# Kernel optimization log

Hardware: AMD Instinct MI355X
Metric: run time of the kernel (lower is better)

Reference implementation:

```python
import jax, jax.numpy as jnp
import numpy as np

NUM_NODES = 100000
HIDDEN = 128
NUM_EDGES = 800000


def setup_inputs() -> dict:
    key = jax.random.key(0)
    ks = jax.random.split(key, 8)
    s = 1.0 / np.sqrt(HIDDEN)

    def lin_w(k):
        return jax.random.uniform(k, (HIDDEN, HIDDEN), minval=-s, maxval=s, dtype=jnp.float32)

    return {
        "node_id": jnp.arange(NUM_NODES, dtype=jnp.int64) if jax.config.jax_enable_x64 else jnp.arange(NUM_NODES, dtype=jnp.int32),
        "edge_index": jax.random.randint(ks[0], (2, NUM_EDGES), 0, NUM_NODES),
        "emb": jax.random.normal(ks[1], (NUM_NODES, HIDDEN), dtype=jnp.float32),
        "W1l": lin_w(ks[2]), "b1l": jnp.zeros((HIDDEN,), jnp.float32), "W1r": lin_w(ks[3]),
        "W2l": lin_w(ks[4]), "b2l": jnp.zeros((HIDDEN,), jnp.float32), "W2r": lin_w(ks[5]),
        "W3l": lin_w(ks[6]), "b3l": jnp.zeros((HIDDEN,), jnp.float32), "W3r": lin_w(ks[7]),
    }


def reference(node_id, edge_index, emb, W1l, b1l, W1r, W2l, b2l, W2r, W3l, b3l, W3r):
    # x: [N, H] node features from embedding lookup
    x = emb[node_id]
    src, dst = edge_index[0], edge_index[1]

    # in-degree per target node (PyG mean aggregation; zero-degree -> 0 output)
    deg = jax.ops.segment_sum(jnp.ones((NUM_EDGES,), x.dtype), dst, num_segments=NUM_NODES)
    inv_deg = 1.0 / jnp.maximum(deg, 1.0)  # [N]

    def sage_conv(h, Wl, bl, Wr):
        # gather source features [E, H], scatter-sum at targets, then mean
        aggr = jax.ops.segment_sum(h[src], dst, num_segments=NUM_NODES) * inv_deg[:, None]
        # out = lin_l(aggr) + lin_r(h); lin_l has bias, lin_r has none (PyG defaults)
        return aggr @ Wl.T + bl + h @ Wr.T

    x = jax.nn.relu(sage_conv(x, W1l, b1l, W1r))
    # dropout p=0.2 with training=False is identity (eval mode)
    x = jax.nn.relu(sage_conv(x, W2l, b2l, W2r))
    return sage_conv(x, W3l, b3l, W3r)
```

## Files before the change

kernel.cpp:

```cpp
#include <hip/hip_runtime.h>

#define H 128

typedef float v4f __attribute__((ext_vector_type(4)));
typedef short v8s __attribute__((ext_vector_type(8)));


__device__ inline unsigned short bf16_rne(float x) {
  unsigned u = __builtin_bit_cast(unsigned, x);
  unsigned r = u + 0x7FFF + ((u >> 16) & 1);
  return (unsigned short)(r >> 16);
}

__device__ inline void split_bf16(float x, unsigned short& hi, unsigned short& lo) {
  unsigned u = __builtin_bit_cast(unsigned, x);
  unsigned r = u + 0x7FFF + ((u >> 16) & 1);
  hi = (unsigned short)(r >> 16);
  float hf = __builtin_bit_cast(float, r & 0xFFFF0000u);
  float d = x - hf;
  unsigned ud = __builtin_bit_cast(unsigned, d);
  unsigned rd = ud + 0x7FFF + ((ud >> 16) & 1);
  lo = (unsigned short)(rd >> 16);
}


__global__ void hist_kernel(const int* __restrict__ dst, int* __restrict__ deg, int E) {
  int e = blockIdx.x * 256 + threadIdx.x;
  if (e < E) atomicAdd(&deg[dst[e]], 1);
}

__global__ __launch_bounds__(1024) void scan1_kernel(const int* __restrict__ deg,
                                                     int* __restrict__ incl,
                                                     int* __restrict__ blk_sum, int N) {
  __shared__ int lds[1024];
  int t = threadIdx.x;
  int i = blockIdx.x * 1024 + t;
  int v = (i < N) ? deg[i] : 0;
  lds[t] = v;
  __syncthreads();
  for (int off = 1; off < 1024; off <<= 1) {
    int x = (t >= off) ? lds[t - off] : 0;
    __syncthreads();
    lds[t] += x;
    __syncthreads();
  }
  if (i < N) incl[i] = lds[t];
  if (t == 1023) blk_sum[blockIdx.x] = lds[1023];
}

__global__ void scan2_kernel(const int* __restrict__ blk_sum, int* __restrict__ blk_off, int B) {
  __shared__ int lds[256];
  int t = threadIdx.x;
  int v = (t < B) ? blk_sum[t] : 0;
  lds[t] = v;
  __syncthreads();
  for (int off = 1; off < 256; off <<= 1) {
    int x = (t >= off) ? lds[t - off] : 0;
    __syncthreads();
    lds[t] += x;
    __syncthreads();
  }
  blk_off[t] = lds[t] - v;
}

__global__ void rowstart_kernel(const int* __restrict__ incl, const int* __restrict__ deg,
                                const int* __restrict__ blk_off, int* __restrict__ row_start,
                                int N) {
  int i = blockIdx.x * 256 + threadIdx.x;
  if (i < N) row_start[i] = blk_off[i >> 10] + incl[i] - deg[i];
}

__global__ void fill_kernel(const int* __restrict__ src, const int* __restrict__ dst,
                            const int* __restrict__ row_start, int* __restrict__ cursor,
                            int* __restrict__ csr_src, int E) {
  int e = blockIdx.x * 256 + threadIdx.x;
  if (e < E) {
    int d = dst[e];
    int p = atomicAdd(&cursor[d], 1);
    csr_src[row_start[d] + p] = src[e];
  }
}


__global__ void gather_kernel(const float* __restrict__ emb, const int* __restrict__ node_id,
                              float* __restrict__ h, unsigned short* __restrict__ hb, int N) {
  int i = blockIdx.x * 256 + threadIdx.x;
  if (i < N * 32) {
    int n = i >> 5, q = i & 31;
    float4 v = ((const float4*)emb)[(size_t)node_id[n] * 32 + q];
    ((float4*)h)[(size_t)n * 32 + q] = v;
    unsigned b0 = bf16_rne(v.x), b1 = bf16_rne(v.y), b2 = bf16_rne(v.z), b3 = bf16_rne(v.w);
    *(uint2*)(hb + (size_t)n * H + q * 4) = make_uint2(b0 | (b1 << 16), b2 | (b3 << 16));
  }
}


__global__ void wsplit_kernel(const float* __restrict__ W0, const float* __restrict__ W1,
                              const float* __restrict__ W2, const float* __restrict__ W3,
                              const float* __restrict__ W4, const float* __restrict__ W5,
                              unsigned short* __restrict__ hi, unsigned short* __restrict__ lo) {
  int i = blockIdx.x * 256 + threadIdx.x;
  int plane = i >> 12;
  int e = (i & 4095) * 4;
  const float* src = plane == 0 ? W0 : plane == 1 ? W1 : plane == 2 ? W2
                   : plane == 3 ? W3 : plane == 4 ? W4 : W5;
  float4 v = *(const float4*)(src + e);
  float vv[4] = {v.x, v.y, v.z, v.w};
  unsigned short hs[4], ls[4];
#pragma unroll
  for (int k = 0; k < 4; ++k) split_bf16(vv[k], hs[k], ls[k]);
  size_t base = (size_t)plane * 16384 + e;
  *(uint2*)(&hi[base]) = make_uint2((unsigned)hs[0] | ((unsigned)hs[1] << 16),
                                    (unsigned)hs[2] | ((unsigned)hs[3] << 16));
  *(uint2*)(&lo[base]) = make_uint2((unsigned)ls[0] | ((unsigned)ls[1] << 16),
                                    (unsigned)ls[2] | ((unsigned)ls[3] << 16));
}


__global__ __launch_bounds__(256) void aggregate_kernel(const unsigned short* __restrict__ hb,
                                                        const int* __restrict__ csr_src,
                                                        const int* __restrict__ row_start,
                                                        const int* __restrict__ deg,
                                                        float* __restrict__ aggr, int N) {
  int node = blockIdx.x * 4 + (threadIdx.x >> 6);
  if (node >= N) return;
  int lane = threadIdx.x & 63;
  int qe = lane >> 4;
  int cl = lane & 15;
  const uint4* __restrict__ h16 = (const uint4*)hb;

  int start = row_start[node];
  int d = deg[node];

  float acc[8] = {0.f, 0.f, 0.f, 0.f, 0.f, 0.f, 0.f, 0.f};

  auto accum = [&](uint4 u) {
    unsigned uu[4] = {u.x, u.y, u.z, u.w};
#pragma unroll
    for (int j = 0; j < 4; ++j) {
      acc[2 * j] += __builtin_bit_cast(float, uu[j] << 16);
      acc[2 * j + 1] += __builtin_bit_cast(float, uu[j] & 0xFFFF0000u);
    }
  };

  int e = qe;
  for (; e + 4 < d; e += 8) {
    int s0 = csr_src[start + e];
    int s1 = csr_src[start + e + 4];
    uint4 u0 = h16[(size_t)s0 * 16 + cl];
    uint4 u1 = h16[(size_t)s1 * 16 + cl];
    accum(u0);
    accum(u1);
  }
  for (; e < d; e += 4) {
    int s = csr_src[start + e];
    accum(h16[(size_t)s * 16 + cl]);
  }

#pragma unroll
  for (int j = 0; j < 8; ++j) {
    acc[j] += __shfl_xor(acc[j], 16);
    acc[j] += __shfl_xor(acc[j], 32);
  }

  float inv = 1.0f / fmaxf((float)d, 1.0f);
  if (qe == 0) {
    *(float4*)(aggr + (size_t)node * H + cl * 8) =
        make_float4(acc[0] * inv, acc[1] * inv, acc[2] * inv, acc[3] * inv);
  } else if (qe == 1) {
    *(float4*)(aggr + (size_t)node * H + cl * 8 + 4) =
        make_float4(acc[4] * inv, acc[5] * inv, acc[6] * inv, acc[7] * inv);
  }
}


template <int RELU>
__global__ __launch_bounds__(256) void gemm_mfma(const float* __restrict__ aggr,
                                                 const float* h,
                                                 const unsigned short* __restrict__ Wl_hi,
                                                 const unsigned short* __restrict__ Wl_lo,
                                                 const unsigned short* __restrict__ Wr_hi,
                                                 const unsigned short* __restrict__ Wr_lo,
                                                 const float* __restrict__ bias,
                                                 float* out, unsigned short* hb_out, int N) {
  __shared__ __align__(16) unsigned short Ah[4096];
  __shared__ __align__(16) unsigned short Al[4096];
  __shared__ __align__(16) unsigned short Wh[4096];
  __shared__ __align__(16) unsigned short Wl_[4096];

  int tid = threadIdx.x;
  int wave = tid >> 6, lane = tid & 63;
  int m = lane & 15, q = lane >> 4;
  int block_row = blockIdx.x * 128;

  v4f acc[16];
#pragma unroll
  for (int t = 0; t < 16; ++t) acc[t] = (v4f){0.f, 0.f, 0.f, 0.f};

  for (int side = 0; side < 2; ++side) {
    const float* X = side ? h : aggr;
    const unsigned short* WH = side ? Wr_hi : Wl_hi;
    const unsigned short* WL = side ? Wr_lo : Wl_lo;

    for (int kb = 0; kb < 4; ++kb) {
      __syncthreads();

#pragma unroll
      for (int p = 0; p < 4; ++p) {
        int s = p * 256 + tid;
        int row = s >> 3;
        int g = s & 7;
        int grow = block_row + row;
        if (grow >= N) grow = N - 1;
        float4 v = *(const float4*)(X + (size_t)grow * H + kb * 32 + g * 4);
        float vv[4] = {v.x, v.y, v.z, v.w};
        unsigned short hs[4], ls[4];
#pragma unroll
        for (int k = 0; k < 4; ++k) split_bf16(vv[k], hs[k], ls[k]);
        int off = (row >> 4) * 512 + (((g >> 1) * 16) + (row & 15)) * 8 + (g & 1) * 4;
        *(uint2*)(&Ah[off]) = make_uint2((unsigned)hs[0] | ((unsigned)hs[1] << 16),
                                         (unsigned)hs[2] | ((unsigned)hs[3] << 16));
        *(uint2*)(&Al[off]) = make_uint2((unsigned)ls[0] | ((unsigned)ls[1] << 16),
                                         (unsigned)ls[2] | ((unsigned)ls[3] << 16));
      }

#pragma unroll
      for (int p = 0; p < 2; ++p) {
        int s = p * 256 + tid;
        int row = s >> 2;
        int g2 = s & 3;
        size_t gsrc = (size_t)row * H + kb * 32 + g2 * 8;
        v8s wh = *(const v8s*)(WH + gsrc);
        v8s wl = *(const v8s*)(WL + gsrc);
        int off = (row >> 4) * 512 + (g2 * 16 + (row & 15)) * 8;
        *(v8s*)(&Wh[off]) = wh;
        *(v8s*)(&Wl_[off]) = wl;
      }

      __syncthreads();

      const v8s* AhF = (const v8s*)Ah;
      const v8s* AlF = (const v8s*)Al;
      const v8s* WhF = (const v8s*)Wh;
      const v8s* WlF = (const v8s*)Wl_;
      v8s ah0 = AhF[(wave * 2 + 0) * 64 + lane];
      v8s ah1 = AhF[(wave * 2 + 1) * 64 + lane];
      v8s al0 = AlF[(wave * 2 + 0) * 64 + lane];
      v8s al1 = AlF[(wave * 2 + 1) * 64 + lane];
#pragma unroll
      for (int c = 0; c < 8; ++c) {
        v8s bh = WhF[c * 64 + lane];
        v8s bl = WlF[c * 64 + lane];
        acc[c] = __builtin_amdgcn_mfma_f32_16x16x32_bf16(ah0, bh, acc[c], 0, 0, 0);
        acc[c] = __builtin_amdgcn_mfma_f32_16x16x32_bf16(al0, bh, acc[c], 0, 0, 0);
        acc[c] = __builtin_amdgcn_mfma_f32_16x16x32_bf16(ah0, bl, acc[c], 0, 0, 0);
        acc[8 + c] = __builtin_amdgcn_mfma_f32_16x16x32_bf16(ah1, bh, acc[8 + c], 0, 0, 0);
        acc[8 + c] = __builtin_amdgcn_mfma_f32_16x16x32_bf16(al1, bh, acc[8 + c], 0, 0, 0);
        acc[8 + c] = __builtin_amdgcn_mfma_f32_16x16x32_bf16(ah1, bl, acc[8 + c], 0, 0, 0);
      }
    }
  }

  float bv[8];
#pragma unroll
  for (int c = 0; c < 8; ++c) bv[c] = bias[c * 16 + m];
#pragma unroll
  for (int tr = 0; tr < 2; ++tr) {
#pragma unroll
    for (int c = 0; c < 8; ++c) {
      v4f a = acc[tr * 8 + c];
#pragma unroll
      for (int i = 0; i < 4; ++i) {
        int row = block_row + wave * 32 + tr * 16 + q * 4 + i;
        if (row < N) {
          float v = a[i] + bv[c];
          if (RELU) v = fmaxf(v, 0.f);
          out[(size_t)row * H + c * 16 + m] = v;
          if (hb_out) hb_out[(size_t)row * H + c * 16 + m] = bf16_rne(v);
        }
      }
    }
  }
}


extern "C" void kernel_launch(void* const* d_in, const int* in_sizes, int n_in,
                              void* d_out, int out_size, void* d_ws, size_t ws_size,
                              hipStream_t stream) {
  const int* node_id = (const int*)d_in[0];
  const int* edge_index = (const int*)d_in[1];
  const float* emb = (const float*)d_in[2];
  const float* W1l = (const float*)d_in[3];
  const float* b1l = (const float*)d_in[4];
  const float* W1r = (const float*)d_in[5];
  const float* W2l = (const float*)d_in[6];
  const float* b2l = (const float*)d_in[7];
  const float* W2r = (const float*)d_in[8];
  const float* W3l = (const float*)d_in[9];
  const float* b3l = (const float*)d_in[10];
  const float* W3r = (const float*)d_in[11];

  int N = in_sizes[0];
  int E = in_sizes[1] / 2;
  const int* src = edge_index;
  const int* dst = edge_index + E;

  char* w = (char*)d_ws;
  auto alloc = [&](size_t bytes) {
    void* p = (void*)w;
    w += (bytes + 255) & ~(size_t)255;
    return p;
  };
  int* deg = (int*)alloc((size_t)N * 4);
  int* cursor = (int*)alloc((size_t)N * 4);
  int* row_start = (int*)alloc((size_t)N * 4);
  int* incl = (int*)alloc((size_t)N * 4);
  int* blk_sum = (int*)alloc(1024);
  int* blk_off = (int*)alloc(1024);
  int* csr_src = (int*)alloc((size_t)E * 4);
  float* hbuf = (float*)alloc((size_t)N * H * 4);
  float* aggr = (float*)alloc((size_t)N * H * 4);
  unsigned short* hb = (unsigned short*)alloc((size_t)N * H * 2);
  unsigned short* whi = (unsigned short*)alloc(6 * 16384 * 2);
  unsigned short* wlo = (unsigned short*)alloc(6 * 16384 * 2);

  hipMemsetAsync(deg, 0, (size_t)N * 4, stream);
  hipMemsetAsync(cursor, 0, (size_t)N * 4, stream);

  hist_kernel<<<(E + 255) / 256, 256, 0, stream>>>(dst, deg, E);
  int SB = (N + 1023) / 1024;
  scan1_kernel<<<SB, 1024, 0, stream>>>(deg, incl, blk_sum, N);
  scan2_kernel<<<1, 256, 0, stream>>>(blk_sum, blk_off, SB);
  rowstart_kernel<<<(N + 255) / 256, 256, 0, stream>>>(incl, deg, blk_off, row_start, N);
  fill_kernel<<<(E + 255) / 256, 256, 0, stream>>>(src, dst, row_start, cursor, csr_src, E);

  gather_kernel<<<(N * 32 + 255) / 256, 256, 0, stream>>>(emb, node_id, hbuf, hb, N);
  wsplit_kernel<<<96, 256, 0, stream>>>(W1l, W1r, W2l, W2r, W3l, W3r, whi, wlo);

  int gag = (N + 3) / 4;
  int ggm = (N + 127) / 128;

  aggregate_kernel<<<gag, 256, 0, stream>>>(hb, csr_src, row_start, deg, aggr, N);
  gemm_mfma<1><<<ggm, 256, 0, stream>>>(aggr, hbuf, whi + 0 * 16384, wlo + 0 * 16384,
                                        whi + 1 * 16384, wlo + 1 * 16384, b1l, hbuf, hb, N);

  aggregate_kernel<<<gag, 256, 0, stream>>>(hb, csr_src, row_start, deg, aggr, N);
  gemm_mfma<1><<<ggm, 256, 0, stream>>>(aggr, hbuf, whi + 2 * 16384, wlo + 2 * 16384,
                                        whi + 3 * 16384, wlo + 3 * 16384, b2l, hbuf, hb, N);

  aggregate_kernel<<<gag, 256, 0, stream>>>(hb, csr_src, row_start, deg, aggr, N);
  gemm_mfma<0><<<ggm, 256, 0, stream>>>(aggr, hbuf, whi + 4 * 16384, wlo + 4 * 16384,
                                        whi + 5 * 16384, wlo + 5 * 16384, b3l, (float*)d_out,
                                        nullptr, N);
}
```

Baseline: 472.1 us.

## Keep activations as bf16 hi/lo planes and use persistent LDS-resident-weight GEMM

Node features and aggregates are now stored as pre-split bf16 hi/lo planes instead of fp32. The gather, aggregate and GEMM epilogues all perform the split, so the GEMM no longer converts its A operand on the fly. The GEMM becomes a persistent kernel: 256 blocks of 512 threads each load all split weights for the layer into 128KB of dynamic LDS once. Waves then grab 16-row tiles through an atomic counter and double-buffer A fragments straight into registers, which removes per-k-block barriers and repeated weight staging. The costs are heavy register and LDS use, and ping-pong buffers whose output overwrites the aggregate input in place.

```diff
diff --git a/kernel.cpp b/kernel.cpp
--- a/kernel.cpp
+++ b/kernel.cpp
@@ -83,14 +83,21 @@
 
 
 __global__ void gather_kernel(const float* __restrict__ emb, const int* __restrict__ node_id,
-                              float* __restrict__ h, unsigned short* __restrict__ hb, int N) {
+                              unsigned short* __restrict__ h_hi, unsigned short* __restrict__ h_lo,
+                              int N) {
   int i = blockIdx.x * 256 + threadIdx.x;
   if (i < N * 32) {
-    int n = i >> 5, q = i & 31;
-    float4 v = ((const float4*)emb)[(size_t)node_id[n] * 32 + q];
-    ((float4*)h)[(size_t)n * 32 + q] = v;
-    unsigned b0 = bf16_rne(v.x), b1 = bf16_rne(v.y), b2 = bf16_rne(v.z), b3 = bf16_rne(v.w);
-    *(uint2*)(hb + (size_t)n * H + q * 4) = make_uint2(b0 | (b1 << 16), b2 | (b3 << 16));
+    int n = i >> 5, g = i & 31;
+    float4 v = ((const float4*)emb)[(size_t)node_id[n] * 32 + g];
+    float vv[4] = {v.x, v.y, v.z, v.w};
+    unsigned short hs[4], ls[4];
+#pragma unroll
+    for (int k = 0; k < 4; ++k) split_bf16(vv[k], hs[k], ls[k]);
+    size_t base = (size_t)n * H + g * 4;
+    *(uint2*)(h_hi + base) = make_uint2((unsigned)hs[0] | ((unsigned)hs[1] << 16),
+                                        (unsigned)hs[2] | ((unsigned)hs[3] << 16));
+    *(uint2*)(h_lo + base) = make_uint2((unsigned)ls[0] | ((unsigned)ls[1] << 16),
+                                        (unsigned)ls[2] | ((unsigned)ls[3] << 16));
   }
 }
 
@@ -98,22 +105,24 @@
 __global__ void wsplit_kernel(const float* __restrict__ W0, const float* __restrict__ W1,
                               const float* __restrict__ W2, const float* __restrict__ W3,
                               const float* __restrict__ W4, const float* __restrict__ W5,
-                              unsigned short* __restrict__ hi, unsigned short* __restrict__ lo) {
-  int i = blockIdx.x * 256 + threadIdx.x;
-  int plane = i >> 12;
-  int e = (i & 4095) * 4;
-  const float* src = plane == 0 ? W0 : plane == 1 ? W1 : plane == 2 ? W2
-                   : plane == 3 ? W3 : plane == 4 ? W4 : W5;
-  float4 v = *(const float4*)(src + e);
-  float vv[4] = {v.x, v.y, v.z, v.w};
-  unsigned short hs[4], ls[4];
-#pragma unroll
-  for (int k = 0; k < 4; ++k) split_bf16(vv[k], hs[k], ls[k]);
-  size_t base = (size_t)plane * 16384 + e;
-  *(uint2*)(&hi[base]) = make_uint2((unsigned)hs[0] | ((unsigned)hs[1] << 16),
-                                    (unsigned)hs[2] | ((unsigned)hs[3] << 16));
-  *(uint2*)(&lo[base]) = make_uint2((unsigned)ls[0] | ((unsigned)ls[1] << 16),
-                                    (unsigned)ls[2] | ((unsigned)ls[3] << 16));
+                              unsigned short* __restrict__ Wf) {
+  int idx = blockIdx.x * 256 + threadIdx.x;
+  int sp = idx >> 14;
+  int e = idx & 16383;
+  const float* src = sp == 0 ? W0 : sp == 1 ? W1 : sp == 2 ? W2
+                   : sp == 3 ? W3 : sp == 4 ? W4 : W5;
+  int c = e >> 11;
+  int kb = (e >> 9) & 3;
+  int qq = (e >> 7) & 3;
+  int mm = (e >> 3) & 15;
+  int j = e & 7;
+  int col = c * 16 + mm;
+  int k = kb * 32 + qq * 8 + j;
+  unsigned short hi, lo;
+  split_bf16(src[col * H + k], hi, lo);
+  size_t base = (size_t)(sp >> 1) * 65536 + (size_t)(sp & 1) * 32768 + e;
+  Wf[base] = hi;
+  Wf[base + 16384] = lo;
 }
 
 
@@ -121,7 +130,8 @@
                                                         const int* __restrict__ csr_src,
                                                         const int* __restrict__ row_start,
                                                         const int* __restrict__ deg,
-                                                        float* __restrict__ aggr, int N) {
+                                                        unsigned short* __restrict__ a_hi,
+                                                        unsigned short* __restrict__ a_lo, int N) {
   int node = blockIdx.x * 4 + (threadIdx.x >> 6);
   if (node >= N) return;
   int lane = threadIdx.x & 63;
@@ -164,122 +174,126 @@
   }
 
   float inv = 1.0f / fmaxf((float)d, 1.0f);
-  if (qe == 0) {
-    *(float4*)(aggr + (size_t)node * H + cl * 8) =
-        make_float4(acc[0] * inv, acc[1] * inv, acc[2] * inv, acc[3] * inv);
-  } else if (qe == 1) {
-    *(float4*)(aggr + (size_t)node * H + cl * 8 + 4) =
-        make_float4(acc[4] * inv, acc[5] * inv, acc[6] * inv, acc[7] * inv);
-  }
-}
-
-
-template <int RELU>
-__global__ __launch_bounds__(256) void gemm_mfma(const float* __restrict__ aggr,
-                                                 const float* h,
-                                                 const unsigned short* __restrict__ Wl_hi,
-                                                 const unsigned short* __restrict__ Wl_lo,
-                                                 const unsigned short* __restrict__ Wr_hi,
-                                                 const unsigned short* __restrict__ Wr_lo,
-                                                 const float* __restrict__ bias,
-                                                 float* out, unsigned short* hb_out, int N) {
-  __shared__ __align__(16) unsigned short Ah[4096];
-  __shared__ __align__(16) unsigned short Al[4096];
-  __shared__ __align__(16) unsigned short Wh[4096];
-  __shared__ __align__(16) unsigned short Wl_[4096];
-
+  if (qe < 2) {
+    unsigned short hs[4], ls[4];
+    int b = qe * 4;
+#pragma unroll
+    for (int j = 0; j < 4; ++j) split_bf16(acc[b + j] * inv, hs[j], ls[j]);
+    size_t o = (size_t)node * H + cl * 8 + qe * 4;
+    *(uint2*)(a_hi + o) = make_uint2((unsigned)hs[0] | ((unsigned)hs[1] << 16),
+                                     (unsigned)hs[2] | ((unsigned)hs[3] << 16));
+    *(uint2*)(a_lo + o) = make_uint2((unsigned)ls[0] | ((unsigned)ls[1] << 16),
+                                     (unsigned)ls[2] | ((unsigned)ls[3] << 16));
+  }
+}
+
+
+template <int RELU, int FINAL>
+__global__ __launch_bounds__(512, 2) void gemm_ws(
+    const unsigned short* ag_hi, const unsigned short* ag_lo,
+    const unsigned short* h_hi, const unsigned short* h_lo,
+    const unsigned short* __restrict__ Wfrag, const float* __restrict__ bias,
+    unsigned short* out_hi, unsigned short* out_lo, float* __restrict__ outf,
+    int* __restrict__ tcnt, int N) {
+  extern __shared__ unsigned short Wsh[];
   int tid = threadIdx.x;
-  int wave = tid >> 6, lane = tid & 63;
+  {
+    const v8s* gs = (const v8s*)Wfrag;
+    v8s* ls = (v8s*)Wsh;
+#pragma unroll
+    for (int i = 0; i < 16; ++i) ls[tid + i * 512] = gs[tid + i * 512];
+  }
+  int lane = tid & 63;
   int m = lane & 15, q = lane >> 4;
-  int block_row = blockIdx.x * 128;
-
-  v4f acc[16];
-#pragma unroll
-  for (int t = 0; t < 16; ++t) acc[t] = (v4f){0.f, 0.f, 0.f, 0.f};
-
-  for (int side = 0; side < 2; ++side) {
-    const float* X = side ? h : aggr;
-    const unsigned short* WH = side ? Wr_hi : Wl_hi;
-    const unsigned short* WL = side ? Wr_lo : Wl_lo;
-
+  float bv[8];
+#pragma unroll
+  for (int c = 0; c < 8; ++c) bv[c] = bias[c * 16 + m];
+  __syncthreads();
+
+  const v8s* WF = (const v8s*)Wsh;
+  int nT = (N + 15) >> 4;
+
+  auto grab = [&]() {
+    int t = 0;
+    if (lane == 0) t = atomicAdd(tcnt, 1);
+    return __shfl(t, 0);
+  };
+
+  auto loadA = [&](v8s (&a)[16], int t) {
+    int rr = t * 16 + m;
+    if (rr >= N) rr = N - 1;
+    const unsigned short* p0 = ag_hi + (size_t)rr * H + q * 8;
+    const unsigned short* p1 = ag_lo + (size_t)rr * H + q * 8;
+    const unsigned short* p2 = h_hi + (size_t)rr * H + q * 8;
+    const unsigned short* p3 = h_lo + (size_t)rr * H + q * 8;
+#pragma unroll
     for (int kb = 0; kb < 4; ++kb) {
-      __syncthreads();
-
-#pragma unroll
-      for (int p = 0; p < 4; ++p) {
-        int s = p * 256 + tid;
-        int row = s >> 3;
-        int g = s & 7;
-        int grow = block_row + row;
-        if (grow >= N) grow = N - 1;
-        float4 v = *(const float4*)(X + (size_t)grow * H + kb * 32 + g * 4);
-        float vv[4] = {v.x, v.y, v.z, v.w};
-        unsigned short hs[4], ls[4];
-#pragma unroll
-        for (int k = 0; k < 4; ++k) split_bf16(vv[k], hs[k], ls[k]);
-        int off = (row >> 4) * 512 + (((g >> 1) * 16) + (row & 15)) * 8 + (g & 1) * 4;
-        *(uint2*)(&Ah[off]) = make_uint2((unsigned)hs[0] | ((unsigned)hs[1] << 16),
-                                         (unsigned)hs[2] | ((unsigned)hs[3] << 16));
-        *(uint2*)(&Al[off]) = make_uint2((unsigned)ls[0] | ((unsigned)ls[1] << 16),
-                                         (unsigned)ls[2] | ((unsigned)ls[3] << 16));
-      }
-
-#pragma unroll
-      for (int p = 0; p < 2; ++p) {
-        int s = p * 256 + tid;
-        int row = s >> 2;
-        int g2 = s & 3;
-        size_t gsrc = (size_t)row * H + kb * 32 + g2 * 8;
-        v8s wh = *(const v8s*)(WH + gsrc);
-        v8s wl = *(const v8s*)(WL + gsrc);
-        int off = (row >> 4) * 512 + (g2 * 16 + (row & 15)) * 8;
-        *(v8s*)(&Wh[off]) = wh;
-        *(v8s*)(&Wl_[off]) = wl;
-      }
-
-      __syncthreads();
-
-      const v8s* AhF = (const v8s*)Ah;
-      const v8s* AlF = (const v8s*)Al;
-      const v8s* WhF = (const v8s*)Wh;
-      const v8s* WlF = (const v8s*)Wl_;
-      v8s ah0 = AhF[(wave * 2 + 0) * 64 + lane];
-      v8s ah1 = AhF[(wave * 2 + 1) * 64 + lane];
-      v8s al0 = AlF[(wave * 2 + 0) * 64 + lane];
-      v8s al1 = AlF[(wave * 2 + 1) * 64 + lane];
-#pragma unroll
-      for (int c = 0; c < 8; ++c) {
-        v8s bh = WhF[c * 64 + lane];
-        v8s bl = WlF[c * 64 + lane];
-        acc[c] = __builtin_amdgcn_mfma_f32_16x16x32_bf16(ah0, bh, acc[c], 0, 0, 0);
-        acc[c] = __builtin_amdgcn_mfma_f32_16x16x32_bf16(al0, bh, acc[c], 0, 0, 0);
-        acc[c] = __builtin_amdgcn_mfma_f32_16x16x32_bf16(ah0, bl, acc[c], 0, 0, 0);
-        acc[8 + c] = __builtin_amdgcn_mfma_f32_16x16x32_bf16(ah1, bh, acc[8 + c], 0, 0, 0);
-        acc[8 + c] = __builtin_amdgcn_mfma_f32_16x16x32_bf16(al1, bh, acc[8 + c], 0, 0, 0);
-        acc[8 + c] = __builtin_amdgcn_mfma_f32_16x16x32_bf16(ah1, bl, acc[8 + c], 0, 0, 0);
-      }
+      a[kb] = *(const v8s*)(p0 + kb * 32);
+      a[4 + kb] = *(const v8s*)(p1 + kb * 32);
+      a[8 + kb] = *(const v8s*)(p2 + kb * 32);
+      a[12 + kb] = *(const v8s*)(p3 + kb * 32);
     }
-  }
-
-  float bv[8];
-#pragma unroll
-  for (int c = 0; c < 8; ++c) bv[c] = bias[c * 16 + m];
-#pragma unroll
-  for (int tr = 0; tr < 2; ++tr) {
-#pragma unroll
-    for (int c = 0; c < 8; ++c) {
-      v4f a = acc[tr * 8 + c];
-#pragma unroll
-      for (int i = 0; i < 4; ++i) {
-        int row = block_row + wave * 32 + tr * 16 + q * 4 + i;
-        if (row < N) {
-          float v = a[i] + bv[c];
-          if (RELU) v = fmaxf(v, 0.f);
-          out[(size_t)row * H + c * 16 + m] = v;
-          if (hb_out) hb_out[(size_t)row * H + c * 16 + m] = bf16_rne(v);
+  };
+
+  auto computeStore = [&](const v8s (&a)[16], int t) {
+    v4f acc[8];
+#pragma unroll
+    for (int c = 0; c < 8; ++c) acc[c] = (v4f){0.f, 0.f, 0.f, 0.f};
+#pragma unroll
+    for (int s = 0; s < 2; ++s) {
+#pragma unroll
+      for (int kb = 0; kb < 4; ++kb) {
+        v8s ah = a[s * 8 + kb];
+        v8s al = a[s * 8 + 4 + kb];
+#pragma unroll
+        for (int c = 0; c < 8; ++c) {
+          v8s bh = WF[s * 4096 + c * 256 + kb * 64 + lane];
+          v8s bl = WF[s * 4096 + 2048 + c * 256 + kb * 64 + lane];
+          acc[c] = __builtin_amdgcn_mfma_f32_16x16x32_bf16(ah, bh, acc[c], 0, 0, 0);
+          acc[c] = __builtin_amdgcn_mfma_f32_16x16x32_bf16(al, bh, acc[c], 0, 0, 0);
+          acc[c] = __builtin_amdgcn_mfma_f32_16x16x32_bf16(ah, bl, acc[c], 0, 0, 0);
         }
       }
     }
+#pragma unroll
+    for (int c = 0; c < 8; ++c) {
+#pragma unroll
+      for (int i = 0; i < 4; ++i) {
+        int r = t * 16 + q * 4 + i;
+        if (r < N) {
+          float v = acc[c][i] + bv[c];
+          if (RELU) v = fmaxf(v, 0.f);
+          size_t o = (size_t)r * H + c * 16 + m;
+          if (FINAL) {
+            outf[o] = v;
+          } else {
+            unsigned short hi, lo;
+            split_bf16(v, hi, lo);
+            out_hi[o] = hi;
+            out_lo[o] = lo;
+          }
+        }
+      }
+    }
+  };
+
+  v8s A0[16], A1[16];
+  int tc = grab();
+  if (tc >= nT) return;
+  loadA(A0, tc);
+  int tn = grab();
+  if (tn < nT) loadA(A1, tn);
+  while (true) {
+    computeStore(A0, tc);
+    if (tn >= nT) return;
+    tc = tn;
+    tn = grab();
+    if (tn < nT) loadA(A0, tn);
+    computeStore(A1, tc);
+    if (tn >= nT) return;
+    tc = tn;
+    tn = grab();
+    if (tn < nT) loadA(A1, tn);
   }
 }
 
@@ -318,14 +332,25 @@
   int* blk_sum = (int*)alloc(1024);
   int* blk_off = (int*)alloc(1024);
   int* csr_src = (int*)alloc((size_t)E * 4);
-  float* hbuf = (float*)alloc((size_t)N * H * 4);
-  float* aggr = (float*)alloc((size_t)N * H * 4);
-  unsigned short* hb = (unsigned short*)alloc((size_t)N * H * 2);
-  unsigned short* whi = (unsigned short*)alloc(6 * 16384 * 2);
-  unsigned short* wlo = (unsigned short*)alloc(6 * 16384 * 2);
+  int* tcnt = (int*)alloc(256);
+  unsigned short* P0h = (unsigned short*)alloc((size_t)N * H * 2);
+  unsigned short* P0l = (unsigned short*)alloc((size_t)N * H * 2);
+  unsigned short* P1h = (unsigned short*)alloc((size_t)N * H * 2);
+  unsigned short* P1l = (unsigned short*)alloc((size_t)N * H * 2);
+  unsigned short* Wf = (unsigned short*)alloc((size_t)3 * 65536 * 2);
+
+  static int attr_done = 0;
+  if (!attr_done) {
+    hipFuncSetAttribute(reinterpret_cast<const void*>(&gemm_ws<1, 0>),
+                        hipFuncAttributeMaxDynamicSharedMemorySize, 131072);
+    hipFuncSetAttribute(reinterpret_cast<const void*>(&gemm_ws<0, 1>),
+                        hipFuncAttributeMaxDynamicSharedMemorySize, 131072);
+    attr_done = 1;
+  }
 
   hipMemsetAsync(deg, 0, (size_t)N * 4, stream);
   hipMemsetAsync(cursor, 0, (size_t)N * 4, stream);
+  hipMemsetAsync(tcnt, 0, 256, stream);
 
   hist_kernel<<<(E + 255) / 256, 256, 0, stream>>>(dst, deg, E);
   int SB = (N + 1023) / 1024;
@@ -334,22 +359,20 @@
   rowstart_kernel<<<(N + 255) / 256, 256, 0, stream>>>(incl, deg, blk_off, row_start, N);
   fill_kernel<<<(E + 255) / 256, 256, 0, stream>>>(src, dst, row_start, cursor, csr_src, E);
 
-  gather_kernel<<<(N * 32 + 255) / 256, 256, 0, stream>>>(emb, node_id, hbuf, hb, N);
-  wsplit_kernel<<<96, 256, 0, stream>>>(W1l, W1r, W2l, W2r, W3l, W3r, whi, wlo);
+  gather_kernel<<<(N * 32 + 255) / 256, 256, 0, stream>>>(emb, node_id, P0h, P0l, N);
+  wsplit_kernel<<<384, 256, 0, stream>>>(W1l, W1r, W2l, W2r, W3l, W3r, Wf);
 
   int gag = (N + 3) / 4;
-  int ggm = (N + 127) / 128;
-
-  aggregate_kernel<<<gag, 256, 0, stream>>>(hb, csr_src, row_start, deg, aggr, N);
-  gemm_mfma<1><<<ggm, 256, 0, stream>>>(aggr, hbuf, whi + 0 * 16384, wlo + 0 * 16384,
-                                        whi + 1 * 16384, wlo + 1 * 16384, b1l, hbuf, hb, N);
-
-  aggregate_kernel<<<gag, 256, 0, stream>>>(hb, csr_src, row_start, deg, aggr, N);
-  gemm_mfma<1><<<ggm, 256, 0, stream>>>(aggr, hbuf, whi + 2 * 16384, wlo + 2 * 16384,
-                                        whi + 3 * 16384, wlo + 3 * 16384, b2l, hbuf, hb, N);
-
-  aggregate_kernel<<<gag, 256, 0, stream>>>(hb, csr_src, row_start, deg, aggr, N);
-  gemm_mfma<0><<<ggm, 256, 0, stream>>>(aggr, hbuf, whi + 4 * 16384, wlo + 4 * 16384,
-                                        whi + 5 * 16384, wlo + 5 * 16384, b3l, (float*)d_out,
-                                        nullptr, N);
-}
+
+  aggregate_kernel<<<gag, 256, 0, stream>>>(P0h, csr_src, row_start, deg, P1h, P1l, N);
+  gemm_ws<1, 0><<<256, 512, 131072, stream>>>(P1h, P1l, P0h, P0l, Wf, b1l,
+                                              P1h, P1l, nullptr, tcnt, N);
+
+  aggregate_kernel<<<gag, 256, 0, stream>>>(P1h, csr_src, row_start, deg, P0h, P0l, N);
+  gemm_ws<1, 0><<<256, 512, 131072, stream>>>(P0h, P0l, P1h, P1l, Wf + 65536, b2l,
+                                              P0h, P0l, nullptr, tcnt + 1, N);
+
+  aggregate_kernel<<<gag, 256, 0, stream>>>(P0h, csr_src, row_start, deg, P1h, P1l, N);
+  gemm_ws<0, 1><<<256, 512, 131072, stream>>>(P1h, P1l, P0h, P0l, Wf + 131072, b3l,
+                                              nullptr, nullptr, (float*)d_out, tcnt + 2, N);
+}
```

Result: slower. 821.9 us (+74.1%).
